# Kernel optimization log

Hardware: AMD Instinct MI355X
Metric: run time of the kernel (lower is better)

Reference implementation:

```python
import jax, jax.numpy as jnp
import numpy as np

T, B, I, H = 32, 16, 512, 512
OFF = 441  # triu diagonal offset from get_sparse_config(512,512,0.99) -> 2556 coeffs


def _idct_weight(N):
    # Ortho DCT-II matrix C[k,n]; the idct DCTLayer weight is C^T so that
    # linear(x) = x @ (C^T)^T = x @ C = idct_ortho(x).
    n = np.arange(N)
    C = np.sqrt(2.0 / N) * np.cos(np.pi * (2 * n[None, :] + 1) * n[:, None] / (2 * N))
    C[0] /= np.sqrt(2.0)
    return jnp.asarray(C.T, dtype=jnp.float32)


def setup_inputs() -> dict:
    key = jax.random.key(0)
    ks = jax.random.split(key, 8)
    rows_np, cols_np = np.triu_indices(H, OFF, I)
    NC = rows_np.shape[0]  # 2556

    def u(k, shape, fan):
        s = 1.0 / np.sqrt(fan)
        return jax.random.uniform(k, shape, jnp.float32, -s, s)

    return {
        "input_": jax.random.normal(ks[0], (T, B, I), jnp.float32),
        # coefficient-generating LSTMs (torch nn.LSTM(input_dim, n_coeffs)),
        # b = b_ih + b_hh folded into one bias (mathematically identical)
        "wih_ih": u(ks[1], (4 * NC, I), NC),
        "wih_hh": u(ks[2], (4 * NC, NC), NC),
        "wih_b": u(ks[3], (4 * NC,), NC),
        "whh_ih": u(ks[4], (4 * NC, I), NC),
        "whh_hh": u(ks[5], (4 * NC, NC), NC),
        "whh_b": u(ks[6], (4 * NC,), NC),
        "coef_scaler_ih": jnp.ones((NC,), jnp.float32),
        "coef_scaler_hh": jnp.ones((NC,), jnp.float32),
        "bias": u(ks[7], (H,), H),
        "idct_in": _idct_weight(I),
        "idct_hid": _idct_weight(H),
        "rows": jnp.asarray(rows_np, jnp.int32),
        "cols": jnp.asarray(cols_np, jnp.int32),
    }


def _lstm(x_seq, Wih, Whh, b):
    # Standard torch LSTM, gate order i,f,g,o. x_seq: [T,B,in]
    C = Whh.shape[-1]

    def step(carry, x):
        h, c = carry
        g = x @ Wih.T + h @ Whh.T + b
        i, f, gg, o = jnp.split(g, 4, axis=-1)
        c = jax.nn.sigmoid(f) * c + jax.nn.sigmoid(i) * jnp.tanh(gg)
        h = jax.nn.sigmoid(o) * jnp.tanh(c)
        return (h, c), h

    h0 = jnp.zeros((x_seq.shape[1], C), x_seq.dtype)
    _, hs = jax.lax.scan(step, (h0, h0), x_seq)
    return hs  # [T,B,C]


def _reconstruct(coeffs, rows, cols, A, Bm, out_dim, in_dim):
    # scatter sparse DCT coeffs into upper-diagonal band, flip left-right,
    # then 2D inverse DCT via two dense matmuls: W = Bm @ fliplr(S) @ A^T
    S = jnp.zeros((coeffs.shape[0], out_dim, in_dim), coeffs.dtype)
    S = S.at[:, rows, cols].set(coeffs)
    Sf = S[:, :, ::-1]
    return jnp.einsum('hk,bki,ji->bhj', Bm, Sf, A)  # [b,out_dim,in_dim]


def _forward(input_, wih_ih, wih_hh, wih_b, whh_ih, whh_hh, whh_b,
             coef_scaler_ih, coef_scaler_hh, bias, idct_in, idct_hid, rows, cols):
    coeffs_ih = _lstm(input_, wih_ih, wih_hh, wih_b) * coef_scaler_ih  # [T,B,NC]
    coeffs_hh = _lstm(input_, whh_ih, whh_hh, whh_b) * coef_scaler_hh

    def step(h, inp):
        x, cih, chh = inp
        Wih = _reconstruct(cih, rows, cols, idct_in, idct_hid, H, I)   # [B,H,I]
        Whh = _reconstruct(chh, rows, cols, idct_hid, idct_hid, H, H)  # [B,H,H]
        h = jnp.tanh(jnp.einsum('bi,bhi->bh', x, Wih)
                     + jnp.einsum('bj,bhj->bh', h, Whh) + bias)
        return h, h

    h0 = jnp.zeros((input_.shape[1], H), input_.dtype)
    _, out = jax.lax.scan(step, h0, (input_, coeffs_ih, coeffs_hh))
    return out  # [T,B,H]


def reference(input_, wih_ih, wih_hh, wih_b, whh_ih, whh_hh, whh_b,
              coef_scaler_ih, coef_scaler_hh, bias, idct_in, idct_hid, rows, cols):
    return _forward(input_, wih_ih, wih_hh, wih_b, whh_ih, whh_hh, whh_b,
                    coef_scaler_ih, coef_scaler_hh, bias, idct_in, idct_hid, rows, cols)
```

## Files before the change

kernel.cpp:

```cpp
#include <hip/hip_runtime.h>
#include <hip/hip_bf16.h>

#define T_ 32
#define B_ 16
#define I_ 512
#define H_ 512
#define OFF_ 441
#define NR_ 71
#define NC_ 2556
#define G4_ (4*NC_)
#define NCP_ 2560
#define NPR_ 10240
#define NTIL_ 640

typedef __attribute__((ext_vector_type(8))) short bf16x8;
typedef __attribute__((ext_vector_type(4))) float f32x4;
typedef __attribute__((ext_vector_type(4))) int   i32x4;

__device__ __forceinline__ ushort bfc(float f) {
    __hip_bfloat16 h = __float2bfloat16(f);
    return *(ushort*)&h;
}
__device__ __forceinline__ float b2f(ushort u) {
    return __uint_as_float((uint)u << 16);
}
__device__ __forceinline__ float sigf(float x) { return 1.f / (1.f + expf(-x)); }

__global__ void k_zero(float* __restrict__ p, int n) {
    int i = blockIdx.x * 256 + threadIdx.x;
    if (i < n) p[i] = 0.f;
}

__global__ void k_cvt_x(const float* __restrict__ x, ushort* __restrict__ xb) {
    int i = blockIdx.x * 256 + threadIdx.x;
    float4 v = ((const float4*)x)[i];
    ushort4 o; o.x = bfc(v.x); o.y = bfc(v.y); o.z = bfc(v.z); o.w = bfc(v.w);
    ((ushort4*)xb)[i] = o;
}

__global__ void k_cvt_w512p(const float* __restrict__ W0, const float* __restrict__ W1,
                            ushort* __restrict__ dst) {
    int l = blockIdx.z;
    const float* src = l ? W1 : W0;
    size_t idx = (size_t)blockIdx.x * 256 + threadIdx.x;
    int np = (int)(idx >> 7), kq = (int)(idx & 127);
    ushort4 o; o.x = 0; o.y = 0; o.z = 0; o.w = 0;
    int jc = np >> 2, q = np & 3;
    if (jc < NC_) {
        float4 v = *(const float4*)(src + ((size_t)q * NC_ + jc) * I_ + kq * 4);
        o.x = bfc(v.x); o.y = bfc(v.y); o.z = bfc(v.z); o.w = bfc(v.w);
    }
    ((ushort4*)(dst + ((size_t)l * NPR_ + np) * I_))[kq] = o;
}

__global__ __launch_bounds__(256) void k_cvt_whh_i8(const float* __restrict__ W0,
        const float* __restrict__ W1,
        signed char* __restrict__ dst, float* __restrict__ sW) {
    const int l = blockIdx.z;
    const float* src = l ? W1 : W0;
    const int np = blockIdx.x * 4 + (threadIdx.x >> 6);
    const int lane = threadIdx.x & 63;
    const int jc = np >> 2, q = np & 3;
    float w[40];
    float mx = 0.f;
    if (jc < NC_) {
        const float* row = src + ((size_t)q * NC_ + jc) * NC_;
        #pragma unroll
        for (int g = 0; g < 5; ++g) {
            int k0 = g * 512 + lane * 8;
            #pragma unroll
            for (int e = 0; e < 8; ++e) {
                int k = k0 + e;
                float v = (k < NC_) ? row[k] : 0.f;
                w[g * 8 + e] = v;
                mx = fmaxf(mx, fabsf(v));
            }
        }
    } else {
        #pragma unroll
        for (int i = 0; i < 40; ++i) w[i] = 0.f;
    }
    #pragma unroll
    for (int d = 1; d < 64; d <<= 1) mx = fmaxf(mx, __shfl_xor(mx, d));
    const float inv = (mx > 0.f) ? 127.f / mx : 0.f;
    const int nt = np >> 4, r = np & 15;
    signed char* obase = dst + (((size_t)l * NTIL_ + nt) * 40) * 1024;
    #pragma unroll
    for (int g = 0; g < 5; ++g) {
        int k0 = g * 512 + lane * 8;
        int ks = k0 >> 6, kgrp = (k0 >> 4) & 3, e = k0 & 15;
        uint lo = 0, hi = 0;
        #pragma unroll
        for (int ee = 0; ee < 4; ++ee) {
            lo |= ((uint)(uchar)(signed char)(int)rintf(w[g * 8 + ee] * inv)) << (8 * ee);
            hi |= ((uint)(uchar)(signed char)(int)rintf(w[g * 8 + 4 + ee] * inv)) << (8 * ee);
        }
        *(uint2*)(obase + (size_t)ks * 1024 + (kgrp * 16 + r) * 16 + e) = make_uint2(lo, hi);
    }
    if (lane == 0) sW[(size_t)l * NPR_ + np] = (mx > 0.f) ? mx / 127.f : 0.f;
}

__global__ __launch_bounds__(256) void k_gih_mfma(const ushort* __restrict__ Xbf,
        const ushort* __restrict__ Wp,
        const float* __restrict__ b0, const float* __restrict__ b1,
        ushort* __restrict__ preT) {
    const int l = blockIdx.z;
    const float* bb = l ? b1 : b0;
    const int wid = threadIdx.x >> 6, lane = threadIdx.x & 63;
    const int nt = blockIdx.x * 4 + wid;
    __shared__ ushort lds_a[32 * 64 * 8];
    const int srow = lane & 15, skq = (lane >> 4) * 8;
    const ushort* wp = Wp + ((size_t)l * NPR_ + nt * 16 + srow) * I_ + skq;
    f32x4 acc[32];
    #pragma unroll
    for (int mt = 0; mt < 32; ++mt) acc[mt] = (f32x4){0.f, 0.f, 0.f, 0.f};
    for (int ks = 0; ks < 16; ++ks) {
        #pragma unroll
        for (int i = 0; i < 8; ++i) {
            int mt = wid * 8 + i;
            bf16x8 xv = *(const bf16x8*)(Xbf + (size_t)(mt * 16 + srow) * I_ + ks * 32 + skq);
            *(bf16x8*)(lds_a + (mt * 64 + lane) * 8) = xv;
        }
        bf16x8 b = *(const bf16x8*)(wp + ks * 32);
        __syncthreads();
        #pragma unroll
        for (int mt = 0; mt < 32; ++mt) {
            bf16x8 a = *(const bf16x8*)(lds_a + (mt * 64 + lane) * 8);
            acc[mt] = __builtin_amdgcn_mfma_f32_16x16x32_bf16(a, b, acc[mt], 0, 0, 0);
        }
        __syncthreads();
    }
    const int n = nt * 16 + srow;
    const float bv = (n < G4_) ? bb[(size_t)(n & 3) * NC_ + (n >> 2)] : 0.f;
    const int r0 = (lane >> 4) * 4;
    ushort* po = preT + ((size_t)l * NPR_ + n) * 512;
    #pragma unroll
    for (int mt = 0; mt < 32; ++mt) {
        ushort4 o;
        o.x = bfc(acc[mt][0] + bv); o.y = bfc(acc[mt][1] + bv);
        o.z = bfc(acc[mt][2] + bv); o.w = bfc(acc[mt][3] + bv);
        *(ushort4*)(po + mt * 16 + r0) = o;
    }
}

__global__ __launch_bounds__(256, 4) void k_step(const signed char* __restrict__ Wq8,
        const float* __restrict__ sW, const ushort* __restrict__ preT,
        const signed char* __restrict__ h_in, signed char* __restrict__ h_out,
        float* __restrict__ cst, float* __restrict__ hbuf,
        const float* __restrict__ scal_ih, const float* __restrict__ scal_hh,
        int t) {
    const int l = blockIdx.z;
    const int nt0 = blockIdx.x * 2;
    const int tid = threadIdx.x;
    const int w = tid >> 6, lane = tid & 63;
    float pv[4], swv[4];
    const int item_g = tid >> 6;
    const int b_g = tid & 15, jq_g = (tid >> 4) & 3;
    const int nt_g = nt0 + item_g;
    const int jc_g = nt_g * 4 + jq_g;
    if (tid < 128) {
        #pragma unroll
        for (int q = 0; q < 4; ++q) {
            const int row = nt_g * 16 + jq_g * 4 + q;
            pv[q]  = b2f(preT[((size_t)l * NPR_ + row) * 512 + t * 16 + b_g]);
            swv[q] = sW[(size_t)l * NPR_ + row] * (1.f / 127.f);
        }
    }
    const signed char* wbase = Wq8 + (((size_t)l * NTIL_ + nt0) * 40 + w * 10) * 1024 + lane * 16;
    const signed char* hbase = h_in + (size_t)l * 81920 + (w * 10) * 1024 + lane * 16;
    i32x4 s0h = {0, 0, 0, 0}, s0l = {0, 0, 0, 0};
    i32x4 s1h = {0, 0, 0, 0}, s1l = {0, 0, 0, 0};
    #pragma unroll 5
    for (int ks = 0; ks < 10; ++ks) {
        i32x4 ah = *(const i32x4*)(hbase + ks * 1024);
        i32x4 al = *(const i32x4*)(hbase + 40960 + ks * 1024);
        i32x4 b0 = *(const i32x4*)(wbase + ks * 1024);
        i32x4 b1 = *(const i32x4*)(wbase + 40960 + ks * 1024);
        s0h = __builtin_amdgcn_mfma_i32_16x16x64_i8(ah, b0, s0h, 0, 0, 0);
        s0l = __builtin_amdgcn_mfma_i32_16x16x64_i8(al, b0, s0l, 0, 0, 0);
        s1h = __builtin_amdgcn_mfma_i32_16x16x64_i8(ah, b1, s1h, 0, 0, 0);
        s1l = __builtin_amdgcn_mfma_i32_16x16x64_i8(al, b1, s1l, 0, 0, 0);
    }
    __shared__ float gl[2][4][16][17];
    const int col = lane & 15;
    const int m0 = (lane >> 4) * 4;
    #pragma unroll
    for (int v = 0; v < 4; ++v) {
        gl[0][w][col][m0 + v] = (float)s0h[v] + (float)s0l[v] * (1.f / 127.f);
        gl[1][w][col][m0 + v] = (float)s1h[v] + (float)s1l[v] * (1.f / 127.f);
    }
    __syncthreads();
    if (tid < 128 && jc_g < NC_) {
        float g[4];
        #pragma unroll
        for (int q = 0; q < 4; ++q) {
            float s = gl[item_g][0][jq_g * 4 + q][b_g] + gl[item_g][1][jq_g * 4 + q][b_g]
                    + gl[item_g][2][jq_g * 4 + q][b_g] + gl[item_g][3][jq_g * 4 + q][b_g];
            g[q] = s * swv[q] + pv[q];
        }
        float* cp = cst + ((size_t)l * NC_ + jc_g) * B_ + b_g;
        float ci = *cp;
        float cn = sigf(g[1]) * ci + sigf(g[0]) * tanhf(g[2]);
        float hn = sigf(g[3]) * tanhf(cn);
        *cp = cn;
        const int ks = jc_g >> 6, kgrp = (jc_g >> 4) & 3, e = jc_g & 15;
        const size_t off = (size_t)l * 81920 + (size_t)ks * 1024 + (kgrp * 16 + b_g) * 16 + e;
        float t1 = hn * 127.f;
        float fhi = rintf(t1);
        float flo = rintf((t1 - fhi) * 127.f);
        h_out[off]         = (signed char)(int)fhi;
        h_out[off + 40960] = (signed char)(int)flo;
        float sc = (l ? scal_hh : scal_ih)[jc_g];
        hbuf[(((size_t)l * T_ + t) * B_ + b_g) * NC_ + jc_g] = hn * sc;
    }
}

__global__ void k_bt(const float* __restrict__ Bh, float* __restrict__ Bt) {
    int idx = blockIdx.x * 256 + threadIdx.x;
    if (idx < NR_ * H_) {
        int k = idx / H_, h = idx - k * H_;
        Bt[idx] = Bh[(size_t)h * H_ + k];
    }
}

__global__ __launch_bounds__(256) void k_yih(const float* __restrict__ x,
        const float* __restrict__ Ain, const float* __restrict__ Bt,
        const float* __restrict__ hbuf0, float* __restrict__ yih) {
    __shared__ float xl[I_];
    __shared__ float u[NR_];
    __shared__ float v[NR_];
    int tb = blockIdx.x;
    int tid = threadIdx.x;
    xl[tid] = x[(size_t)tb * I_ + tid];
    xl[tid + 256] = x[(size_t)tb * I_ + tid + 256];
    __syncthreads();
    if (tid < NR_) {
        float a = 0.f;
        for (int jj = 0; jj < I_; ++jj) a += Ain[(size_t)jj * I_ + tid] * xl[jj];
        u[tid] = a;
    }
    __syncthreads();
    if (tid < NR_) {
        int k = tid;
        int start = k * NR_ - (k * (k - 1)) / 2;
        int cnt = NR_ - k;
        const float* cf = hbuf0 + (size_t)tb * NC_;
        float a = 0.f;
        for (int m = 0; m < cnt; ++m) a += cf[start + m] * u[cnt - 1 - m];
        v[k] = a;
    }
    __syncthreads();
    for (int h = tid; h < H_; h += 256) {
        float a = 0.f;
        #pragma unroll
        for (int k = 0; k < NR_; ++k) a += Bt[(size_t)k * H_ + h] * v[k];
        yih[(size_t)tb * H_ + h] = a;
    }
}

#define BTP_ 520
__global__ __launch_bounds__(576) void k_seq(const float* __restrict__ yih,
        const float* __restrict__ Bt, const float* __restrict__ cf_all,
        const float* __restrict__ bias, float* __restrict__ out) {
    __shared__ __align__(16) float bt[NR_ * BTP_];
    __shared__ __align__(16) float hl[2][H_];
    __shared__ float u[NR_ + 1];
    __shared__ __align__(16) float v[NR_ + 1];
    const int b = blockIdx.x, tid = threadIdx.x;
    for (int i = tid; i < NR_ * H_; i += 576)
        bt[(i >> 9) * BTP_ + (i & 511)] = Bt[i];
    for (int i = tid; i < H_; i += 576) hl[0][i] = 0.f;
    if (tid == 0) { u[NR_] = 0.f; v[NR_] = 0.f; }
    const float bv = (tid < H_) ? bias[tid] : 0.f;
    const int g = tid >> 3, lane = tid & 7;
    int start = 0, cnt = 0;
    if (g < NR_) { start = g * NR_ - (g * (g - 1)) / 2; cnt = NR_ - g; }
    int p = 0;
    __syncthreads();
    for (int t = 0; t < T_; ++t) {
        float cfv[9];
        if (g < NR_) {
            const float* cf = cf_all + ((size_t)t * B_ + b) * NC_ + start;
            #pragma unroll
            for (int mi = 0; mi < 9; ++mi) {
                int m = mi * 8 + lane;
                cfv[mi] = cf[m < cnt ? m : (cnt - 1)];
            }
        }
        if (g < NR_) {
            const float* bp = bt + g * BTP_ + lane * 4;
            const float* hp = hl[p] + lane * 4;
            float a = 0.f;
            #pragma unroll
            for (int m = 0; m < 16; ++m) {
                float4 bq = *(const float4*)(bp + m * 32);
                float4 hq = *(const float4*)(hp + m * 32);
                a += bq.x * hq.x + bq.y * hq.y + bq.z * hq.z + bq.w * hq.w;
            }
            a += __shfl_xor(a, 1); a += __shfl_xor(a, 2); a += __shfl_xor(a, 4);
            if (lane == 0) u[g] = a;
        }
        __syncthreads();
        if (g < NR_) {
            float a = 0.f;
            #pragma unroll
            for (int mi = 0; mi < 9; ++mi) {
                int m = mi * 8 + lane;
                a += (m < cnt) ? cfv[mi] * u[cnt - 1 - m] : 0.f;
            }
            a += __shfl_xor(a, 1); a += __shfl_xor(a, 2); a += __shfl_xor(a, 4);
            if (lane == 0) v[g] = a;
        }
        __syncthreads();
        if (tid < H_) {
            float4 vv[18];
            #pragma unroll
            for (int q = 0; q < 18; ++q) vv[q] = *(const float4*)(v + q * 4);
            float a0 = 0.f, a1 = 0.f;
            #pragma unroll
            for (int k = 0; k < NR_; ++k) {
                float vk = ((const float*)vv)[k];
                ((k & 1) ? a1 : a0) += bt[k * BTP_ + tid] * vk;
            }
            float hv = tanhf(yih[((size_t)t * B_ + b) * H_ + tid] + a0 + a1 + bv);
            out[((size_t)t * B_ + b) * H_ + tid] = hv;
            hl[p ^ 1][tid] = hv;
        }
        __syncthreads();
        p ^= 1;
    }
}

extern "C" void kernel_launch(void* const* d_in, const int* in_sizes, int n_in,
                              void* d_out, int out_size, void* d_ws, size_t ws_size,
                              hipStream_t stream) {
    const float* x        = (const float*)d_in[0];
    const float* wih_ih   = (const float*)d_in[1];
    const float* wih_hh   = (const float*)d_in[2];
    const float* wih_b    = (const float*)d_in[3];
    const float* whh_ih   = (const float*)d_in[4];
    const float* whh_hh   = (const float*)d_in[5];
    const float* whh_b    = (const float*)d_in[6];
    const float* scal_ih  = (const float*)d_in[7];
    const float* scal_hh  = (const float*)d_in[8];
    const float* bias     = (const float*)d_in[9];
    const float* idct_in  = (const float*)d_in[10];
    const float* idct_hid = (const float*)d_in[11];
    float* out = (float*)d_out;

    const size_t WP8_B  = (size_t)2 * NPR_ * NCP_;
    const size_t SW_B   = (size_t)2 * NPR_ * 4;
    const size_t PRET_B = (size_t)2 * NPR_ * 512 * 2;
    const size_t HBUF_B = (size_t)2 * T_ * B_ * NC_ * 4;
    const size_t HBF_B  = (size_t)2 * 2 * 2 * 40960;
    const size_t CST_B  = (size_t)2 * NC_ * B_ * 4;
    const size_t YIH_B  = (size_t)T_ * B_ * H_ * 4;
    const size_t BT_B   = (size_t)NR_ * H_ * 4;
    const size_t need = WP8_B + SW_B + PRET_B + HBUF_B + HBF_B + CST_B + YIH_B + BT_B + 4096;

    char* ws = (char*)d_ws;
    size_t off = 0;
    auto alloc = [&](size_t bytes) -> void* {
        void* p = (void*)(ws + off);
        off += (bytes + 255) & ~(size_t)255;
        return p;
    };

    if (ws_size < need) return;

    signed char* Wp8 = (signed char*)alloc(WP8_B);
    float*  sW   = (float*)alloc(SW_B);
    ushort* preT = (ushort*)alloc(PRET_B);
    float*  hbuf = (float*)alloc(HBUF_B);
    signed char* hbf = (signed char*)alloc(HBF_B);
    float*  cst  = (float*)alloc(CST_B);
    float*  yih  = (float*)alloc(YIH_B);
    float*  Bt   = (float*)alloc(BT_B);
    ushort* Wih_p = (ushort*)Wp8;
    ushort* Xbf   = (ushort*)((char*)Wp8 + 21000192);

    {
        int n = (int)((HBF_B + CST_B) / 4);
        hipLaunchKernelGGL(k_zero, dim3((n + 255) / 256), dim3(256), 0, stream,
                           (float*)hbf, n);
    }
    hipLaunchKernelGGL(k_cvt_x, dim3(256), dim3(256), 0, stream, x, Xbf);
    hipLaunchKernelGGL(k_cvt_w512p, dim3(NPR_ * 128 / 256, 1, 2), dim3(256), 0, stream,
                       wih_ih, whh_ih, Wih_p);
    hipLaunchKernelGGL(k_gih_mfma, dim3(160, 1, 2), dim3(256), 0, stream,
                       Xbf, Wih_p, wih_b, whh_b, preT);
    hipLaunchKernelGGL(k_cvt_whh_i8, dim3(NPR_ / 4, 1, 2), dim3(256), 0, stream,
                       wih_hh, whh_hh, Wp8, sW);

    const size_t HS = (size_t)2 * 81920;
    for (int t = 0; t < T_; ++t) {
        const signed char* hin  = hbf + (size_t)(t & 1) * HS;
        signed char*       hout = hbf + (size_t)((t & 1) ^ 1) * HS;
        hipLaunchKernelGGL(k_step, dim3(NTIL_ / 2, 1, 2), dim3(256), 0, stream,
                           Wp8, sW, preT, hin, hout, cst, hbuf, scal_ih, scal_hh, t);
    }

    hipLaunchKernelGGL(k_bt, dim3((NR_ * H_ + 255) / 256), dim3(256), 0, stream,
                       idct_hid, Bt);
    hipLaunchKernelGGL(k_yih, dim3(T_ * B_), dim3(256), 0, stream,
                       x, idct_in, Bt, hbuf, yih);
    hipLaunchKernelGGL(k_seq, dim3(B_), dim3(576), 0, stream,
                       yih, Bt, hbuf + (size_t)T_ * B_ * NC_, bias, out);
}
```

Before: 680.0 us.

## Widen LSTM step tiles, parallelize yih projection, prefetch yih in sequential loop

The per-timestep LSTM kernel now has each block process four column tiles instead of two. All four waves do gate work, the h fragments are reused across more weight tiles, and the grid is half as large. k_yih is restructured with a transposed copy of the input IDCT slice, which gives coalesced float4 loads, plus 8-lane cooperative dot products and shuffle reductions, replacing single-thread serial loops. k_seq splits its dot product into more independent accumulators and loads yih early to hide latency. The risks are higher register pressure in k_step, fewer blocks per launch, and an extra transpose kernel.

```diff
diff --git a/kernel.cpp b/kernel.cpp
--- a/kernel.cpp
+++ b/kernel.cpp
@@ -150,7 +150,7 @@
         const float* __restrict__ scal_ih, const float* __restrict__ scal_hh,
         int t) {
     const int l = blockIdx.z;
-    const int nt0 = blockIdx.x * 2;
+    const int nt0 = blockIdx.x * 4;
     const int tid = threadIdx.x;
     const int w = tid >> 6, lane = tid & 63;
     float pv[4], swv[4];
@@ -158,7 +158,7 @@
     const int b_g = tid & 15, jq_g = (tid >> 4) & 3;
     const int nt_g = nt0 + item_g;
     const int jc_g = nt_g * 4 + jq_g;
-    if (tid < 128) {
+    {
         #pragma unroll
         for (int q = 0; q < 4; ++q) {
             const int row = nt_g * 16 + jq_g * 4 + q;
@@ -168,29 +168,30 @@
     }
     const signed char* wbase = Wq8 + (((size_t)l * NTIL_ + nt0) * 40 + w * 10) * 1024 + lane * 16;
     const signed char* hbase = h_in + (size_t)l * 81920 + (w * 10) * 1024 + lane * 16;
-    i32x4 s0h = {0, 0, 0, 0}, s0l = {0, 0, 0, 0};
-    i32x4 s1h = {0, 0, 0, 0}, s1l = {0, 0, 0, 0};
-    #pragma unroll 5
+    i32x4 sh[4], sl[4];
+    #pragma unroll
+    for (int i = 0; i < 4; ++i) { sh[i] = (i32x4){0,0,0,0}; sl[i] = (i32x4){0,0,0,0}; }
+    #pragma unroll 2
     for (int ks = 0; ks < 10; ++ks) {
         i32x4 ah = *(const i32x4*)(hbase + ks * 1024);
         i32x4 al = *(const i32x4*)(hbase + 40960 + ks * 1024);
-        i32x4 b0 = *(const i32x4*)(wbase + ks * 1024);
-        i32x4 b1 = *(const i32x4*)(wbase + 40960 + ks * 1024);
-        s0h = __builtin_amdgcn_mfma_i32_16x16x64_i8(ah, b0, s0h, 0, 0, 0);
-        s0l = __builtin_amdgcn_mfma_i32_16x16x64_i8(al, b0, s0l, 0, 0, 0);
-        s1h = __builtin_amdgcn_mfma_i32_16x16x64_i8(ah, b1, s1h, 0, 0, 0);
-        s1l = __builtin_amdgcn_mfma_i32_16x16x64_i8(al, b1, s1l, 0, 0, 0);
-    }
-    __shared__ float gl[2][4][16][17];
+        #pragma unroll
+        for (int i = 0; i < 4; ++i) {
+            i32x4 bw = *(const i32x4*)(wbase + (size_t)i * 40960 + ks * 1024);
+            sh[i] = __builtin_amdgcn_mfma_i32_16x16x64_i8(ah, bw, sh[i], 0, 0, 0);
+            sl[i] = __builtin_amdgcn_mfma_i32_16x16x64_i8(al, bw, sl[i], 0, 0, 0);
+        }
+    }
+    __shared__ float gl[4][4][16][17];
     const int col = lane & 15;
     const int m0 = (lane >> 4) * 4;
     #pragma unroll
-    for (int v = 0; v < 4; ++v) {
-        gl[0][w][col][m0 + v] = (float)s0h[v] + (float)s0l[v] * (1.f / 127.f);
-        gl[1][w][col][m0 + v] = (float)s1h[v] + (float)s1l[v] * (1.f / 127.f);
-    }
+    for (int i = 0; i < 4; ++i)
+        #pragma unroll
+        for (int v = 0; v < 4; ++v)
+            gl[i][w][col][m0 + v] = (float)sh[i][v] + (float)sl[i][v] * (1.f / 127.f);
     __syncthreads();
-    if (tid < 128 && jc_g < NC_) {
+    if (jc_g < NC_) {
         float g[4];
         #pragma unroll
         for (int q = 0; q < 4; ++q) {
@@ -223,38 +224,72 @@
     }
 }
 
-__global__ __launch_bounds__(256) void k_yih(const float* __restrict__ x,
-        const float* __restrict__ Ain, const float* __restrict__ Bt,
+__global__ void k_at(const float* __restrict__ Ain, float* __restrict__ AinT) {
+    int idx = blockIdx.x * 256 + threadIdx.x;
+    if (idx < NR_ * I_) {
+        int g = idx / I_, j = idx - g * I_;
+        AinT[idx] = Ain[(size_t)j * I_ + g];
+    }
+}
+
+__global__ __launch_bounds__(576) void k_yih(const float* __restrict__ x,
+        const float* __restrict__ AinT, const float* __restrict__ Bt,
         const float* __restrict__ hbuf0, float* __restrict__ yih) {
-    __shared__ float xl[I_];
-    __shared__ float u[NR_];
-    __shared__ float v[NR_];
-    int tb = blockIdx.x;
-    int tid = threadIdx.x;
-    xl[tid] = x[(size_t)tb * I_ + tid];
-    xl[tid + 256] = x[(size_t)tb * I_ + tid + 256];
+    __shared__ __align__(16) float xl[I_];
+    __shared__ float u[NR_ + 1];
+    __shared__ __align__(16) float v[NR_ + 1];
+    const int tb = blockIdx.x, tid = threadIdx.x;
+    for (int i = tid; i < I_; i += 576) xl[i] = x[(size_t)tb * I_ + i];
+    if (tid == 0) { u[NR_] = 0.f; v[NR_] = 0.f; }
+    const int g = tid >> 3, lane = tid & 7;
     __syncthreads();
-    if (tid < NR_) {
+    if (g < NR_) {
+        const float* ap = AinT + (size_t)g * I_ + lane * 4;
+        const float* hp = xl + lane * 4;
+        float4 aq[8], hq[8];
+        float a0 = 0.f, a1 = 0.f, a2 = 0.f, a3 = 0.f;
+        #pragma unroll
+        for (int m = 0; m < 8; ++m) { aq[m] = *(const float4*)(ap + m * 32);
+                                      hq[m] = *(const float4*)(hp + m * 32); }
+        #pragma unroll
+        for (int m = 0; m < 8; ++m) {
+            a0 += aq[m].x * hq[m].x; a1 += aq[m].y * hq[m].y;
+            a2 += aq[m].z * hq[m].z; a3 += aq[m].w * hq[m].w;
+        }
+        #pragma unroll
+        for (int m = 0; m < 8; ++m) { aq[m] = *(const float4*)(ap + (m + 8) * 32);
+                                      hq[m] = *(const float4*)(hp + (m + 8) * 32); }
+        #pragma unroll
+        for (int m = 0; m < 8; ++m) {
+            a0 += aq[m].x * hq[m].x; a1 += aq[m].y * hq[m].y;
+            a2 += aq[m].z * hq[m].z; a3 += aq[m].w * hq[m].w;
+        }
+        float a = (a0 + a1) + (a2 + a3);
+        a += __shfl_xor(a, 1); a += __shfl_xor(a, 2); a += __shfl_xor(a, 4);
+        if (lane == 0) u[g] = a;
+    }
+    __syncthreads();
+    if (g < NR_) {
+        int start = g * NR_ - (g * (g - 1)) / 2;
+        int cnt = NR_ - g;
+        const float* cf = hbuf0 + (size_t)tb * NC_ + start;
         float a = 0.f;
-        for (int jj = 0; jj < I_; ++jj) a += Ain[(size_t)jj * I_ + tid] * xl[jj];
-        u[tid] = a;
+        for (int m = lane; m < cnt; m += 8) a += cf[m] * u[cnt - 1 - m];
+        a += __shfl_xor(a, 1); a += __shfl_xor(a, 2); a += __shfl_xor(a, 4);
+        if (lane == 0) v[g] = a;
     }
     __syncthreads();
-    if (tid < NR_) {
-        int k = tid;
-        int start = k * NR_ - (k * (k - 1)) / 2;
-        int cnt = NR_ - k;
-        const float* cf = hbuf0 + (size_t)tb * NC_;
-        float a = 0.f;
-        for (int m = 0; m < cnt; ++m) a += cf[start + m] * u[cnt - 1 - m];
-        v[k] = a;
-    }
-    __syncthreads();
-    for (int h = tid; h < H_; h += 256) {
-        float a = 0.f;
-        #pragma unroll
-        for (int k = 0; k < NR_; ++k) a += Bt[(size_t)k * H_ + h] * v[k];
-        yih[(size_t)tb * H_ + h] = a;
+    if (tid < H_) {
+        float4 vv[18];
+        #pragma unroll
+        for (int q = 0; q < 18; ++q) vv[q] = *(const float4*)(v + q * 4);
+        float a0 = 0.f, a1 = 0.f;
+        #pragma unroll
+        for (int k = 0; k < NR_; ++k) {
+            float vk = ((const float*)vv)[k];
+            ((k & 1) ? a1 : a0) += Bt[(size_t)k * H_ + tid] * vk;
+        }
+        yih[(size_t)tb * H_ + tid] = a0 + a1;
     }
 }
 
@@ -278,6 +313,8 @@
     int p = 0;
     __syncthreads();
     for (int t = 0; t < T_; ++t) {
+        float yv = 0.f;
+        if (tid < H_) yv = yih[((size_t)t * B_ + b) * H_ + tid];
         float cfv[9];
         if (g < NR_) {
             const float* cf = cf_all + ((size_t)t * B_ + b) * NC_ + start;
@@ -290,13 +327,25 @@
         if (g < NR_) {
             const float* bp = bt + g * BTP_ + lane * 4;
             const float* hp = hl[p] + lane * 4;
-            float a = 0.f;
-            #pragma unroll
-            for (int m = 0; m < 16; ++m) {
-                float4 bq = *(const float4*)(bp + m * 32);
-                float4 hq = *(const float4*)(hp + m * 32);
-                a += bq.x * hq.x + bq.y * hq.y + bq.z * hq.z + bq.w * hq.w;
-            }
+            float4 bq[8], hq[8];
+            float a0 = 0.f, a1 = 0.f, a2 = 0.f, a3 = 0.f;
+            #pragma unroll
+            for (int m = 0; m < 8; ++m) { bq[m] = *(const float4*)(bp + m * 32);
+                                          hq[m] = *(const float4*)(hp + m * 32); }
+            #pragma unroll
+            for (int m = 0; m < 8; ++m) {
+                a0 += bq[m].x * hq[m].x; a1 += bq[m].y * hq[m].y;
+                a2 += bq[m].z * hq[m].z; a3 += bq[m].w * hq[m].w;
+            }
+            #pragma unroll
+            for (int m = 0; m < 8; ++m) { bq[m] = *(const float4*)(bp + (m + 8) * 32);
+                                          hq[m] = *(const float4*)(hp + (m + 8) * 32); }
+            #pragma unroll
+            for (int m = 0; m < 8; ++m) {
+                a0 += bq[m].x * hq[m].x; a1 += bq[m].y * hq[m].y;
+                a2 += bq[m].z * hq[m].z; a3 += bq[m].w * hq[m].w;
+            }
+            float a = (a0 + a1) + (a2 + a3);
             a += __shfl_xor(a, 1); a += __shfl_xor(a, 2); a += __shfl_xor(a, 4);
             if (lane == 0) u[g] = a;
         }
@@ -322,7 +371,7 @@
                 float vk = ((const float*)vv)[k];
                 ((k & 1) ? a1 : a0) += bt[k * BTP_ + tid] * vk;
             }
-            float hv = tanhf(yih[((size_t)t * B_ + b) * H_ + tid] + a0 + a1 + bv);
+            float hv = tanhf(yv + a0 + a1 + bv);
             out[((size_t)t * B_ + b) * H_ + tid] = hv;
             hl[p ^ 1][tid] = hv;
         }
@@ -356,7 +405,8 @@
     const size_t CST_B  = (size_t)2 * NC_ * B_ * 4;
     const size_t YIH_B  = (size_t)T_ * B_ * H_ * 4;
     const size_t BT_B   = (size_t)NR_ * H_ * 4;
-    const size_t need = WP8_B + SW_B + PRET_B + HBUF_B + HBF_B + CST_B + YIH_B + BT_B + 4096;
+    const size_t AT_B   = (size_t)NR_ * I_ * 4;
+    const size_t need = WP8_B + SW_B + PRET_B + HBUF_B + HBF_B + CST_B + YIH_B + BT_B + AT_B + 4096;
 
     char* ws = (char*)d_ws;
     size_t off = 0;
@@ -376,6 +426,7 @@
     float*  cst  = (float*)alloc(CST_B);
     float*  yih  = (float*)alloc(YIH_B);
     float*  Bt   = (float*)alloc(BT_B);
+    float*  AinT = (float*)alloc(AT_B);
     ushort* Wih_p = (ushort*)Wp8;
     ushort* Xbf   = (ushort*)((char*)Wp8 + 21000192);
 
@@ -396,14 +447,16 @@
     for (int t = 0; t < T_; ++t) {
         const signed char* hin  = hbf + (size_t)(t & 1) * HS;
         signed char*       hout = hbf + (size_t)((t & 1) ^ 1) * HS;
-        hipLaunchKernelGGL(k_step, dim3(NTIL_ / 2, 1, 2), dim3(256), 0, stream,
+        hipLaunchKernelGGL(k_step, dim3(NTIL_ / 4, 1, 2), dim3(256), 0, stream,
                            Wp8, sW, preT, hin, hout, cst, hbuf, scal_ih, scal_hh, t);
     }
 
     hipLaunchKernelGGL(k_bt, dim3((NR_ * H_ + 255) / 256), dim3(256), 0, stream,
                        idct_hid, Bt);
-    hipLaunchKernelGGL(k_yih, dim3(T_ * B_), dim3(256), 0, stream,
-                       x, idct_in, Bt, hbuf, yih);
+    hipLaunchKernelGGL(k_at, dim3((NR_ * I_ + 255) / 256), dim3(256), 0, stream,
+                       idct_in, AinT);
+    hipLaunchKernelGGL(k_yih, dim3(T_ * B_), dim3(576), 0, stream,
+                       x, AinT, Bt, hbuf, yih);
     hipLaunchKernelGGL(k_seq, dim3(B_), dim3(576), 0, stream,
                        yih, Bt, hbuf + (size_t)T_ * B_ * NC_, bias, out);
 }
```

After: 786.8 us. 15.7% more time.
